# Optimization experiments

Measured on AMD Instinct MI355X. Metric: run time of the kernel, lower is better.

## Reference

```python
import jax, jax.numpy as jnp
import numpy as np

EPS = 0.5
GAM1 = 1.0
GAM2 = 1.0
GAM3 = 1.0


def setup_inputs() -> dict:
    key = jax.random.key(0)
    k1, k2, k3 = jax.random.split(key, 3)
    n, d, C = 8192, 512, 10
    Z = jax.random.normal(k1, (n, d), dtype=jnp.float32)
    Z_bar = jax.random.normal(k2, (n, d), dtype=jnp.float32)
    real_label = jax.random.randint(k3, (n,), 0, C)
    return {"Z": Z, "Z_bar": Z_bar, "real_label": real_label, "num_classes": C}


def _mcr_terms(Z, Z_bar, real_label, num_classes):
    n, d = Z.shape
    dtype = Z.dtype
    Pi = jax.nn.one_hot(real_label, num_classes, dtype=dtype)  # [n, C]
    counts = Pi.sum(axis=0)                                    # [C]
    I = jnp.eye(d, dtype=dtype)

    # Discriminative terms: logdet(I + d/(n*eps) * Z^T Z) / 2
    disc_z = jnp.linalg.slogdet(I + (d / (n * EPS)) * (Z.T @ Z))[1] / 2.0
    disc_zb = jnp.linalg.slogdet(I + (d / (n * EPS)) * (Z_bar.T @ Z_bar))[1] / 2.0

    # Per-class Grams: Z[:, mask_j] @ Z[:, mask_j].T == Z^T diag(Pi[:,j]) Z
    Gz = jnp.einsum('nc,nd,ne->cde', Pi, Z, Z)          # [C, d, d]
    Gzb = jnp.einsum('nc,nd,ne->cde', Pi, Z_bar, Z_bar)  # [C, d, d]

    trPi = counts + 1e-8                                 # matches torch's +1e-08
    scal = (d / (trPi * EPS))[:, None, None]
    ld_z = jnp.linalg.slogdet(I[None] + scal * Gz)[1]    # raw logdets (not halved)
    ld_zb = jnp.linalg.slogdet(I[None] + scal * Gzb)[1]
    s = trPi / (2.0 * n)
    comp_z = jnp.sum(s * ld_z)
    comp_zb = jnp.sum(s * ld_zb)

    z_total = -(disc_z - comp_z)
    zb_total = -(disc_zb - comp_zb)

    # R(z_j, zbar_j): concat rows -> Gram sum, n_j = 2*count_j (exact count)
    n_j = 2.0 * counts
    scal3 = (d / (n_j * EPS))[:, None, None]
    ld3 = jnp.linalg.slogdet(I[None] + scal3 * (Gz + Gzb))[1] / 2.0
    item = jnp.sum(ld3)

    term3 = item - 0.25 * jnp.sum(ld_z) - 0.25 * jnp.sum(ld_zb)
    errD = -(GAM1 * (disc_z - comp_z) + GAM2 * (disc_zb - comp_zb) + GAM3 * term3)
    return errD, z_total, zb_total, term3


def reference(Z, Z_bar, real_label, num_classes):
    errD, z_total, zb_total, term3 = _mcr_terms(Z, Z_bar, real_label, num_classes)
    # empi = [z_total, zbar_total, term3]; pack everything into one vector
    return jnp.stack([errD, z_total, zb_total, term3])
```

## Files before the change

### kernel.cpp

```cpp
#include <hip/hip_runtime.h>
#include <math.h>

#define NROWS 8192
#define DIM   512
#define NCLS  10
#define GT    4
#define GPAIR 10
#define NMAT  32

__global__ __launch_bounds__(256) void k_count(const int* __restrict__ label,
                                               int* __restrict__ counts,
                                               int* __restrict__ lists) {
    __shared__ int hist[NCLS];
    __shared__ int base[NCLS];
    __shared__ int lofs[NCLS];
    int tid = threadIdx.x;
    int i = blockIdx.x * 256 + tid;
    if (tid < NCLS) { hist[tid] = 0; lofs[tid] = 0; }
    __syncthreads();
    int c = label[i];
    atomicAdd(&hist[c], 1);
    __syncthreads();
    if (tid < NCLS) base[tid] = atomicAdd(&counts[tid], hist[tid]);
    __syncthreads();
    int lpos = atomicAdd(&lofs[c], 1);
    lists[(size_t)c * NROWS + base[c] + lpos] = i;
}

__global__ __launch_bounds__(512) void k_gram(const float* __restrict__ Z,
                                              const float* __restrict__ Zb,
                                              const int* __restrict__ counts,
                                              const int* __restrict__ lists,
                                              float* __restrict__ G) {
    int pt = blockIdx.x;
    int c  = blockIdx.y;
    int tz = blockIdx.z;
    int ti = 0, tj = 0;
    { int p = pt;
      for (int r = 0; r < GT; ++r) { if (p <= r) { ti = r; tj = p; break; } p -= (r + 1); } }
    bool diag = (ti == tj);

    const float* __restrict__ src = tz ? Zb : Z;
    float* __restrict__ Gout = G + (((size_t)tz * NCLS + c) * GPAIR + pt) * 16384;
    int cnt = counts[c];
    const int* __restrict__ list = lists + (size_t)c * NROWS;

    __shared__ float As[2][16][132];
    __shared__ float Bs[2][16][132];
    int tid = threadIdx.x;
    int gid = tid >> 8;
    int t   = tid & 255;
    int tx = t & 15, ty = t >> 4;
    int srow = t >> 4, sc4 = t & 15;

    float acc[8][8];
    #pragma unroll
    for (int r = 0; r < 8; ++r)
        #pragma unroll
        for (int s = 0; s < 8; ++s) acc[r][s] = 0.f;

    for (int base0 = 0; base0 < cnt; base0 += 32) {
        int gr = base0 + gid * 16 + srow;
        float4 va0 = make_float4(0.f, 0.f, 0.f, 0.f), va1 = va0, vb0 = va0, vb1 = va0;
        if (gr < cnt) {
            int ridx = list[gr];
            const float* __restrict__ rp = src + (size_t)ridx * DIM;
            va0 = *(const float4*)&rp[ti * 128 + sc4 * 4];
            va1 = *(const float4*)&rp[ti * 128 + 64 + sc4 * 4];
            if (!diag) {
                vb0 = *(const float4*)&rp[tj * 128 + sc4 * 4];
                vb1 = *(const float4*)&rp[tj * 128 + 64 + sc4 * 4];
            }
        }
        *(float4*)&As[gid][srow][sc4 * 4]      = va0;
        *(float4*)&As[gid][srow][64 + sc4 * 4] = va1;
        if (!diag) {
            *(float4*)&Bs[gid][srow][sc4 * 4]      = vb0;
            *(float4*)&Bs[gid][srow][64 + sc4 * 4] = vb1;
        }
        __syncthreads();

        const float (*__restrict__ Ap)[132] = As[gid];
        const float (*__restrict__ Bp)[132] = diag ? As[gid] : Bs[gid];
        #pragma unroll
        for (int kk = 0; kk < 16; ++kk) {
            float a[8], b[8];
            *(float4*)&a[0] = *(const float4*)&Ap[kk][ty * 4];
            *(float4*)&a[4] = *(const float4*)&Ap[kk][64 + ty * 4];
            *(float4*)&b[0] = *(const float4*)&Bp[kk][tx * 4];
            *(float4*)&b[4] = *(const float4*)&Bp[kk][64 + tx * 4];
            #pragma unroll
            for (int r = 0; r < 8; ++r)
                #pragma unroll
                for (int s = 0; s < 8; ++s)
                    acc[r][s] += a[r] * b[s];
        }
        __syncthreads();
    }

    float* red = (float*)&As[0][0][0];
    #pragma unroll
    for (int r = 0; r < 8; ++r) {
        __syncthreads();
        if (gid == 1) {
            #pragma unroll
            for (int s = 0; s < 8; ++s) red[t * 8 + s] = acc[r][s];
        }
        __syncthreads();
        if (gid == 0) {
            #pragma unroll
            for (int s = 0; s < 8; ++s) acc[r][s] += red[t * 8 + s];
        }
    }
    if (gid == 0) {
        #pragma unroll
        for (int r = 0; r < 8; ++r) {
            int row = (r < 4) ? (ty * 4 + r) : (64 + ty * 4 + r - 4);
            float4 v0 = make_float4(acc[r][0], acc[r][1], acc[r][2], acc[r][3]);
            float4 v1 = make_float4(acc[r][4], acc[r][5], acc[r][6], acc[r][7]);
            *(float4*)&Gout[(size_t)row * 128 + tx * 4]      = v0;
            *(float4*)&Gout[(size_t)row * 128 + 64 + tx * 4] = v1;
        }
    }
}

__global__ __launch_bounds__(256) void k_assemble(const float* __restrict__ G,
                                                  const int* __restrict__ counts,
                                                  float* __restrict__ A) {
    int pt = blockIdx.x;
    int m  = blockIdx.y;
    int ti = 0, tj = 0;
    { int p = pt;
      for (int r = 0; r < GT; ++r) { if (p <= r) { ti = r; tj = p; break; } p -= (r + 1); } }

    const size_t TILE = 16384;
    const float* __restrict__ Gz  = G;
    const float* __restrict__ Gzb = G + (size_t)NCLS * GPAIR * TILE;
    float* __restrict__ Am = A + (size_t)m * DIM * DIM;
    int tid = threadIdx.x;

    int mode; int c; float sc;
    if (m < 10)      { mode = 0; c = m;      sc = 1024.f / ((float)counts[c] + 1e-8f); }
    else if (m < 20) { mode = 1; c = m - 10; sc = 1024.f / ((float)counts[c] + 1e-8f); }
    else if (m < 30) { mode = 2; c = m - 20; sc = 512.f / (float)counts[c]; }
    else             { mode = (m == 30) ? 3 : 4; c = 0; sc = 0.125f; }

    #pragma unroll 1
    for (int h = 0; h < 16; ++h) {
        int id = h * 256 + tid;
        int row = id >> 5, c4 = id & 31;
        size_t off = (size_t)row * 128 + c4 * 4;
        float4 g = make_float4(0.f, 0.f, 0.f, 0.f);
        if (mode == 0) {
            g = *(const float4*)&Gz[((size_t)c * GPAIR + pt) * TILE + off];
        } else if (mode == 1) {
            g = *(const float4*)&Gzb[((size_t)c * GPAIR + pt) * TILE + off];
        } else if (mode == 2) {
            float4 a = *(const float4*)&Gz [((size_t)c * GPAIR + pt) * TILE + off];
            float4 b = *(const float4*)&Gzb[((size_t)c * GPAIR + pt) * TILE + off];
            g.x = a.x + b.x; g.y = a.y + b.y; g.z = a.z + b.z; g.w = a.w + b.w;
        } else if (mode == 3) {
            for (int cc = 0; cc < NCLS; ++cc) {
                float4 t = *(const float4*)&Gz[((size_t)cc * GPAIR + pt) * TILE + off];
                g.x += t.x; g.y += t.y; g.z += t.z; g.w += t.w;
            }
        } else {
            for (int cc = 0; cc < NCLS; ++cc) {
                float4 t = *(const float4*)&Gzb[((size_t)cc * GPAIR + pt) * TILE + off];
                g.x += t.x; g.y += t.y; g.z += t.z; g.w += t.w;
            }
        }
        g.x *= sc; g.y *= sc; g.z *= sc; g.w *= sc;
        if (ti == tj) {
            int cb = c4 * 4;
            if (row == cb)     g.x += 1.f;
            if (row == cb + 1) g.y += 1.f;
            if (row == cb + 2) g.z += 1.f;
            if (row == cb + 3) g.w += 1.f;
        }
        *(float4*)&Am[(size_t)(ti * 128 + row) * DIM + tj * 128 + c4 * 4] = g;
    }
}

__global__ __launch_bounds__(256) void k_panel(float* __restrict__ A,
                                               float* __restrict__ ld,
                                               int p) {
    int K = 7 - p;
    int m    = blockIdx.y;
    int pair = blockIdx.x;
    int a = 0, b = 0;
    { int q = pair;
      for (int r = 0; r < 8; ++r) { if (q <= r) { a = r; b = q; break; } q -= (r + 1); } }

    float* __restrict__ Am = A + (size_t)m * DIM * DIM;
    int col0 = p * 64, col1 = col0 + 64;
    int tid = threadIdx.x;

    __shared__ float Dl[64][65];
    __shared__ float dinv[64];
    __shared__ float Ta[64][68];
    __shared__ float Tb[64][68];

    for (int h = tid; h < 1024; h += 256) {
        int r = h >> 4, c4 = h & 15;
        *(float4*)&Dl[r][c4 * 4] = *(const float4*)&Am[(size_t)(col0 + r) * DIM + col0 + c4 * 4];
    }
    __syncthreads();

    if (tid < 64) {
        int lane = tid;
        float row_[64];
        #pragma unroll
        for (int j = 0; j < 64; ++j) row_[j] = Dl[lane][j];
        float dval = 1.f;
        #pragma unroll
        for (int k = 0; k < 64; ++k) {
            float piv = __shfl(row_[k], k);
            float s = 1.0f / sqrtf(piv);
            float lik = row_[k] * s;
            dval = (lane == k) ? lik : dval;
            row_[k] = lik;
            #pragma unroll
            for (int j = k + 1; j < 64; ++j)
                row_[j] -= lik * __shfl(lik, j);
        }
        #pragma unroll
        for (int j = 0; j < 64; ++j) Dl[lane][j] = row_[j];
        dinv[lane] = 1.f / dval;
        if (pair == 0) {
            float v = 2.f * logf(dval);
            #pragma unroll
            for (int off = 32; off > 0; off >>= 1) v += __shfl_down(v, off);
            if (lane == 0) atomicAdd(&ld[m], v);
        }
    }
    __syncthreads();
    if (K == 0) return;

    int chunk = tid >> 6;
    if (chunk == 0 || (chunk == 1 && b != a)) {
        int which = chunk ? b : a;
        int r = tid & 63;
        const float* __restrict__ Brow = Am + (size_t)(col1 + which * 64 + r) * DIM + col0;
        float (*__restrict__ Tp)[68] = chunk ? Tb : Ta;
        float t[64];
        #pragma unroll
        for (int i = 0; i < 64; ++i) {
            float acc0 = Brow[i], acc1 = 0.f;
            int mm = 0;
            #pragma unroll
            for (; mm + 1 < i; mm += 2) {
                acc0 -= t[mm]     * Dl[i][mm];
                acc1 -= t[mm + 1] * Dl[i][mm + 1];
            }
            if (mm < i) acc0 -= t[mm] * Dl[i][mm];
            t[i] = (acc0 + acc1) * dinv[i];
            Tp[i][r] = t[i];
        }
    }
    __syncthreads();

    int tx = tid & 15, ty = tid >> 4;
    float acc[4][4];
    #pragma unroll
    for (int r = 0; r < 4; ++r)
        #pragma unroll
        for (int s = 0; s < 4; ++s) acc[r][s] = 0.f;
    const float (*__restrict__ TB)[68] = (b == a) ? Ta : Tb;
    #pragma unroll 8
    for (int kk = 0; kk < 64; ++kk) {
        float av[4], bv[4];
        *(float4*)av = *(const float4*)&Ta[kk][ty * 4];
        *(float4*)bv = *(const float4*)&TB[kk][tx * 4];
        #pragma unroll
        for (int r = 0; r < 4; ++r)
            #pragma unroll
            for (int s = 0; s < 4; ++s)
                acc[r][s] += av[r] * bv[s];
    }
    #pragma unroll
    for (int r = 0; r < 4; ++r) {
        size_t off = (size_t)(col1 + a * 64 + ty * 4 + r) * DIM + col1 + b * 64 + tx * 4;
        float4 cv = *(float4*)&Am[off];
        cv.x -= acc[r][0]; cv.y -= acc[r][1]; cv.z -= acc[r][2]; cv.w -= acc[r][3];
        *(float4*)&Am[off] = cv;
    }
}

__global__ void k_final(const float* __restrict__ ld,
                        const int* __restrict__ counts,
                        float* __restrict__ out) {
    if (threadIdx.x == 0 && blockIdx.x == 0) {
        float disc_z  = 0.5f * ld[30];
        float disc_zb = 0.5f * ld[31];
        float comp_z = 0.f, comp_zb = 0.f, sum_ldz = 0.f, sum_ldzb = 0.f, item = 0.f;
        for (int c = 0; c < NCLS; ++c) {
            float trPi = (float)counts[c] + 1e-8f;
            float s = trPi / (2.f * (float)NROWS);
            comp_z  += s * ld[c];
            comp_zb += s * ld[10 + c];
            sum_ldz  += ld[c];
            sum_ldzb += ld[10 + c];
            item += 0.5f * ld[20 + c];
        }
        float term3 = item - 0.25f * sum_ldz - 0.25f * sum_ldzb;
        float z_total  = -(disc_z - comp_z);
        float zb_total = -(disc_zb - comp_zb);
        float errD = -((disc_z - comp_z) + (disc_zb - comp_zb) + term3);
        out[0] = errD; out[1] = z_total; out[2] = zb_total; out[3] = term3;
    }
}

extern "C" void kernel_launch(void* const* d_in, const int* in_sizes, int n_in,
                              void* d_out, int out_size, void* d_ws, size_t ws_size,
                              hipStream_t stream) {
    (void)in_sizes; (void)n_in; (void)out_size; (void)ws_size;
    const float* Z     = (const float*)d_in[0];
    const float* Zb    = (const float*)d_in[1];
    const int*   label = (const int*)d_in[2];

    char* ws = (char*)d_ws;
    int*   counts = (int*)ws;
    float* ld     = (float*)(ws + 64);
    int*   lists  = (int*)(ws + 256);
    float* G      = (float*)(ws + 256 + (size_t)NCLS * NROWS * 4);
    float* A      = G + (size_t)2 * NCLS * GPAIR * 16384;
    float* out    = (float*)d_out;

    hipMemsetAsync(ws, 0, 256, stream);
    k_count<<<NROWS / 256, 256, 0, stream>>>(label, counts, lists);
    k_gram<<<dim3(GPAIR, NCLS, 2), 512, 0, stream>>>(Z, Zb, counts, lists, G);
    k_assemble<<<dim3(GPAIR, NMAT), 256, 0, stream>>>(G, counts, A);
    for (int p = 0; p < 8; ++p) {
        int K = 7 - p;
        int pairs = (K > 0) ? K * (K + 1) / 2 : 1;
        k_panel<<<dim3(pairs, NMAT), 256, 0, stream>>>(A, ld, p);
    }
    k_final<<<1, 64, 0, stream>>>(ld, counts, out);
}
```

Baseline: 601.6 us.

## Fuse per-panel Cholesky launches into one persistent block per matrix

Replaces the eight per-panel k_panel launches with a single k_chol kernel that runs one 512-thread block per matrix and loops over all panels internally. The triangular solve for the off-diagonal panel is done once per panel, one row per thread, and kept in a large LDS buffer. Before, every pair block recomputed it. The trailing update uses 8x8 register tiles spread across waves, and the diagonal factorisation uses readlane instead of shuffles. This removes launch overhead and redundant TRSM work, but leaves only 32 blocks on the whole GPU and needs a large LDS allocation.

After: 675.4 us. 1.12x slower.

```diff
diff --git a/kernel.cpp b/kernel.cpp
--- a/kernel.cpp
+++ b/kernel.cpp
@@ -7,6 +7,10 @@
 #define GT    4
 #define GPAIR 10
 #define NMAT  32
+
+__device__ __forceinline__ float rdlane(float v, int l) {
+    return __int_as_float(__builtin_amdgcn_readlane(__float_as_int(v), l));
+}
 
 __global__ __launch_bounds__(256) void k_count(const int* __restrict__ label,
                                                int* __restrict__ counts,
@@ -182,108 +186,120 @@
     }
 }
 
-__global__ __launch_bounds__(256) void k_panel(float* __restrict__ A,
-                                               float* __restrict__ ld,
-                                               int p) {
-    int K = 7 - p;
-    int m    = blockIdx.y;
-    int pair = blockIdx.x;
-    int a = 0, b = 0;
-    { int q = pair;
-      for (int r = 0; r < 8; ++r) { if (q <= r) { a = r; b = q; break; } q -= (r + 1); } }
-
+__global__ __launch_bounds__(512) void k_chol(float* __restrict__ A,
+                                              float* __restrict__ ld) {
+    int m = blockIdx.x;
     float* __restrict__ Am = A + (size_t)m * DIM * DIM;
-    int col0 = p * 64, col1 = col0 + 64;
     int tid = threadIdx.x;
-
-    __shared__ float Dl[64][65];
+    int wave = tid >> 6, lane6 = tid & 63;
+
+    __shared__ float Dl[64][68];
     __shared__ float dinv[64];
-    __shared__ float Ta[64][68];
-    __shared__ float Tb[64][68];
-
-    for (int h = tid; h < 1024; h += 256) {
-        int r = h >> 4, c4 = h & 15;
-        *(float4*)&Dl[r][c4 * 4] = *(const float4*)&Am[(size_t)(col0 + r) * DIM + col0 + c4 * 4];
-    }
-    __syncthreads();
-
-    if (tid < 64) {
-        int lane = tid;
-        float row_[64];
-        #pragma unroll
-        for (int j = 0; j < 64; ++j) row_[j] = Dl[lane][j];
-        float dval = 1.f;
-        #pragma unroll
-        for (int k = 0; k < 64; ++k) {
-            float piv = __shfl(row_[k], k);
-            float s = 1.0f / sqrtf(piv);
-            float lik = row_[k] * s;
-            dval = (lane == k) ? lik : dval;
-            row_[k] = lik;
-            #pragma unroll
-            for (int j = k + 1; j < 64; ++j)
-                row_[j] -= lik * __shfl(lik, j);
-        }
-        #pragma unroll
-        for (int j = 0; j < 64; ++j) Dl[lane][j] = row_[j];
-        dinv[lane] = 1.f / dval;
-        if (pair == 0) {
+    __shared__ float Tl[64][448];
+
+    #pragma unroll 1
+    for (int p = 0; p < 8; ++p) {
+        int col0 = p * 64, col1 = col0 + 64;
+        int mt = DIM - col1;
+        int K = mt >> 6;
+
+        for (int h = tid; h < 1024; h += 512) {
+            int r = h >> 4, c4 = h & 15;
+            *(float4*)&Dl[r][c4 * 4] = *(const float4*)&Am[(size_t)(col0 + r) * DIM + col0 + c4 * 4];
+        }
+        __syncthreads();
+
+        if (tid < 64) {
+            int lane = tid;
+            float row_[64];
+            #pragma unroll
+            for (int j = 0; j < 64; ++j) row_[j] = Dl[lane][j];
+            float dval = 1.f;
+            #pragma unroll
+            for (int k = 0; k < 64; ++k) {
+                float piv = rdlane(row_[k], k);
+                float s = 1.0f / sqrtf(piv);
+                float lik = row_[k] * s;
+                dval = (lane == k) ? lik : dval;
+                row_[k] = lik;
+                #pragma unroll
+                for (int j = k + 1; j < 64; ++j)
+                    row_[j] -= lik * rdlane(lik, j);
+            }
+            #pragma unroll
+            for (int j = 0; j < 64; ++j) Dl[lane][j] = row_[j];
+            dinv[lane] = 1.f / dval;
             float v = 2.f * logf(dval);
             #pragma unroll
             for (int off = 32; off > 0; off >>= 1) v += __shfl_down(v, off);
             if (lane == 0) atomicAdd(&ld[m], v);
         }
-    }
-    __syncthreads();
-    if (K == 0) return;
-
-    int chunk = tid >> 6;
-    if (chunk == 0 || (chunk == 1 && b != a)) {
-        int which = chunk ? b : a;
-        int r = tid & 63;
-        const float* __restrict__ Brow = Am + (size_t)(col1 + which * 64 + r) * DIM + col0;
-        float (*__restrict__ Tp)[68] = chunk ? Tb : Ta;
-        float t[64];
-        #pragma unroll
-        for (int i = 0; i < 64; ++i) {
-            float acc0 = Brow[i], acc1 = 0.f;
-            int mm = 0;
-            #pragma unroll
-            for (; mm + 1 < i; mm += 2) {
-                acc0 -= t[mm]     * Dl[i][mm];
-                acc1 -= t[mm + 1] * Dl[i][mm + 1];
-            }
-            if (mm < i) acc0 -= t[mm] * Dl[i][mm];
-            t[i] = (acc0 + acc1) * dinv[i];
-            Tp[i][r] = t[i];
-        }
-    }
-    __syncthreads();
-
-    int tx = tid & 15, ty = tid >> 4;
-    float acc[4][4];
-    #pragma unroll
-    for (int r = 0; r < 4; ++r)
-        #pragma unroll
-        for (int s = 0; s < 4; ++s) acc[r][s] = 0.f;
-    const float (*__restrict__ TB)[68] = (b == a) ? Ta : Tb;
-    #pragma unroll 8
-    for (int kk = 0; kk < 64; ++kk) {
-        float av[4], bv[4];
-        *(float4*)av = *(const float4*)&Ta[kk][ty * 4];
-        *(float4*)bv = *(const float4*)&TB[kk][tx * 4];
-        #pragma unroll
-        for (int r = 0; r < 4; ++r)
-            #pragma unroll
-            for (int s = 0; s < 4; ++s)
-                acc[r][s] += av[r] * bv[s];
-    }
-    #pragma unroll
-    for (int r = 0; r < 4; ++r) {
-        size_t off = (size_t)(col1 + a * 64 + ty * 4 + r) * DIM + col1 + b * 64 + tx * 4;
-        float4 cv = *(float4*)&Am[off];
-        cv.x -= acc[r][0]; cv.y -= acc[r][1]; cv.z -= acc[r][2]; cv.w -= acc[r][3];
-        *(float4*)&Am[off] = cv;
+        __syncthreads();
+
+        if (tid < mt) {
+            const float* __restrict__ Brow = Am + (size_t)(col1 + tid) * DIM + col0;
+            float t[64];
+            float4 bv;
+            #pragma unroll
+            for (int i = 0; i < 64; ++i) {
+                if ((i & 3) == 0) bv = *(const float4*)&Brow[i];
+                float a0 = (i & 3) == 0 ? bv.x : ((i & 3) == 1 ? bv.y : ((i & 3) == 2 ? bv.z : bv.w));
+                float a1 = 0.f, a2 = 0.f, a3 = 0.f;
+                int mm = 0;
+                #pragma unroll
+                for (; mm + 3 < i; mm += 4) {
+                    float4 d = *(const float4*)&Dl[i][mm];
+                    a0 -= t[mm]     * d.x;
+                    a1 -= t[mm + 1] * d.y;
+                    a2 -= t[mm + 2] * d.z;
+                    a3 -= t[mm + 3] * d.w;
+                }
+                #pragma unroll
+                for (; mm < i; ++mm) a0 -= t[mm] * Dl[i][mm];
+                t[i] = ((a0 + a1) + (a2 + a3)) * dinv[i];
+                Tl[i][tid] = t[i];
+            }
+        }
+        __syncthreads();
+
+        if (K > 0) {
+            int ly = lane6 >> 3, lx = lane6 & 7;
+            int npair = K * (K + 1) / 2;
+            for (int tix = wave; tix < npair; tix += 8) {
+                int a = 0, b = 0;
+                { int q = tix;
+                  for (int r0 = 0; r0 < 7; ++r0) { if (q <= r0) { a = r0; b = q; break; } q -= (r0 + 1); } }
+                float acc[8][8];
+                #pragma unroll
+                for (int r = 0; r < 8; ++r)
+                    #pragma unroll
+                    for (int s = 0; s < 8; ++s) acc[r][s] = 0.f;
+                #pragma unroll 4
+                for (int k = 0; k < 64; ++k) {
+                    float av[8], bv2[8];
+                    *(float4*)&av[0]  = *(const float4*)&Tl[k][a * 64 + ly * 8];
+                    *(float4*)&av[4]  = *(const float4*)&Tl[k][a * 64 + ly * 8 + 4];
+                    *(float4*)&bv2[0] = *(const float4*)&Tl[k][b * 64 + lx * 8];
+                    *(float4*)&bv2[4] = *(const float4*)&Tl[k][b * 64 + lx * 8 + 4];
+                    #pragma unroll
+                    for (int r = 0; r < 8; ++r)
+                        #pragma unroll
+                        for (int s = 0; s < 8; ++s)
+                            acc[r][s] += av[r] * bv2[s];
+                }
+                #pragma unroll
+                for (int r = 0; r < 8; ++r) {
+                    size_t off = (size_t)(col1 + a * 64 + ly * 8 + r) * DIM + col1 + b * 64 + lx * 8;
+                    float4 c0 = *(float4*)&Am[off];
+                    float4 c1 = *(float4*)&Am[off + 4];
+                    c0.x -= acc[r][0]; c0.y -= acc[r][1]; c0.z -= acc[r][2]; c0.w -= acc[r][3];
+                    c1.x -= acc[r][4]; c1.y -= acc[r][5]; c1.z -= acc[r][6]; c1.w -= acc[r][7];
+                    *(float4*)&Am[off]     = c0;
+                    *(float4*)&Am[off + 4] = c1;
+                }
+            }
+        }
+        __syncthreads();
     }
 }
 
@@ -331,10 +347,6 @@
     k_count<<<NROWS / 256, 256, 0, stream>>>(label, counts, lists);
     k_gram<<<dim3(GPAIR, NCLS, 2), 512, 0, stream>>>(Z, Zb, counts, lists, G);
     k_assemble<<<dim3(GPAIR, NMAT), 256, 0, stream>>>(G, counts, A);
-    for (int p = 0; p < 8; ++p) {
-        int K = 7 - p;
-        int pairs = (K > 0) ? K * (K + 1) / 2 : 1;
-        k_panel<<<dim3(pairs, NMAT), 256, 0, stream>>>(A, ld, p);
-    }
+    k_chol<<<NMAT, 512, 0, stream>>>(A, ld);
     k_final<<<1, 64, 0, stream>>>(ld, counts, out);
 }
```
